# Performance work log

Measured on AMD Instinct MI355X. Metric: run time of the kernel, lower is better.

Reference implementation:

```python
import jax, jax.numpy as jnp
import numpy as np

B, N, D, OUT, NUM_ITERS = 8, 4096, 1024, 1024, 3
LN_EPS = 1e-5


def setup_inputs() -> dict:
    key = jax.random.key(0)
    ks = jax.random.split(key, 8)
    s = (6.0 / (2 * D)) ** 0.5  # xavier-uniform-like scale
    return {
        "query": jax.random.normal(ks[0], (B, D), jnp.float32),
        "feat": jax.random.normal(ks[1], (B, N, D), jnp.float32),
        "W_h": jax.random.uniform(ks[2], (D, D), jnp.float32, -s, s),
        "W_f": jax.random.uniform(ks[3], (D, D), jnp.float32, -s, s),
        "W_g": jax.random.normal(ks[4], (4, D, D), jnp.float32) / np.sqrt(D),
        "ln_w": jnp.ones((D,), jnp.float32),
        "ln_b": jnp.zeros((D,), jnp.float32),
        "W_out": jax.random.uniform(ks[5], (OUT, D), jnp.float32, -s, s),
        "b_out": jnp.zeros((OUT,), jnp.float32),
        "feat_mask": jax.random.bernoulli(ks[6], 0.2, (B, 1, 1, N)),
    }


def _layer_norm(x, w, b):
    mu = x.mean(-1, keepdims=True)
    var = jnp.var(x, axis=-1, keepdims=True)
    return (x - mu) / jnp.sqrt(var + LN_EPS) * w + b


def reference(query, feat, W_h, W_f, W_g, ln_w, ln_b, W_out, b_out, feat_mask):
    q = query @ W_h                       # [B, D]
    f = feat @ W_f                        # [B, N, D]
    mask = feat_mask.reshape(feat.shape[0], feat.shape[1])  # squeeze(1).squeeze(1)
    b = jnp.where(mask, jnp.float32(-1e18), jnp.float32(0.0))  # [B, N]
    # feat_group is iteration-invariant: mean over the 4 orthogonal transforms
    # mean_g(f @ W_g[g].T) == f @ mean_g(W_g).T
    fg = f @ W_g.mean(0).T                # [B, N, D]
    n = fg.shape[1]
    for i in range(NUM_ITERS):
        c = jax.nn.softmax(b, axis=1)     # [B, N]
        if i == NUM_ITERS - 1:
            out = jnp.einsum('bn,bnd->bd', c, fg)
        else:
            delta = jnp.einsum('bd,bnd->bn', q, fg)
            delta = (delta - delta.mean(1, keepdims=True)) / (
                delta.std(1, keepdims=True, ddof=1) + 1e-9)  # torch.std is unbiased
            b = b + delta
            out = jnp.einsum('bn,bnd->bd', c, fg) / n  # mean over dim 1
        q = _layer_norm(q + jax.nn.selu(out), ln_w, ln_b)
    return q @ W_out.T + b_out
```

## Files before the change

### kernel.cpp

```cpp
#include <hip/hip_runtime.h>
#include <hip/hip_bf16.h>


using u16 = unsigned short;
using u32 = unsigned int;
using u8  = unsigned char;
using u64 = unsigned long long;

#define SELU_L 1.0507009873554805f
#define SELU_A 1.6732632423543772f

__device__ float g_M[1048576];
__device__ float g_q[8192];
__device__ float g_tus[24576];
__device__ float g_bst[32768];
__device__ float g_c[32768];
__device__ float g_delta[32768];
__device__ float g_outv[8192];
__device__ float g_v[8192];
__device__ int   g_dt[12];

__device__ __forceinline__ float blo(u32 u){ return __uint_as_float(u << 16); }
__device__ __forceinline__ float bhi(u32 u){ return __uint_as_float(u & 0xffff0000u); }
__device__ __forceinline__ float b2f(u16 u){ return __uint_as_float(((u32)u) << 16); }

__device__ __forceinline__ void unpack8(uint4 x, float* f){
  f[0]=blo(x.x); f[1]=bhi(x.x); f[2]=blo(x.y); f[3]=bhi(x.y);
  f[4]=blo(x.z); f[5]=bhi(x.z); f[6]=blo(x.w); f[7]=bhi(x.w);
}

__device__ __forceinline__ float ldf(const void* p, size_t i, int dt){
  return dt ? ((const float*)p)[i] : b2f(((const u16*)p)[i]);
}
__device__ __forceinline__ void load8(const void* base, size_t idx, int dt, float* f){
  if (dt == 0) {
    uint4 x = *(const uint4*)((const u16*)base + idx);
    unpack8(x, f);
  } else {
    const float* p = (const float*)base + idx;
    float4 a = *(const float4*)p, b = *(const float4*)(p + 4);
    f[0]=a.x; f[1]=a.y; f[2]=a.z; f[3]=a.w; f[4]=b.x; f[5]=b.y; f[6]=b.z; f[7]=b.w;
  }
}

__device__ __forceinline__ float wredsum(float x){
#pragma unroll
  for (int o = 32; o; o >>= 1) x += __shfl_xor(x, o, 64);
  return x;
}

__global__ void kdet(const void* p0, const void* p1, const void* p2, const void* p3,
                     const void* p4, const void* p5, const void* p6, const void* p7,
                     const void* p8, const void* p9)
{
  const void* ps[10] = {p0,p1,p2,p3,p4,p5,p6,p7,p8,p9};
  int tid = threadIdx.x;
  int w = tid >> 6, lane = tid & 63;
  if (w < 9) {
    const u16* wp = (const u16*)ps[w];
    u16 x0 = wp[lane], x1 = wp[64 + lane];
    int e0 = (x0 >> 7) & 0xFF, e1 = (x1 >> 7) & 0xFF;
    u64 nz0 = __ballot(x0 != 0), nz1 = __ballot(x1 != 0);
    u64 pa0 = __ballot(x0 != 0 && e0 >= 0x70 && e0 <= 0x8F);
    u64 pa1 = __ballot(x1 != 0 && e1 >= 0x70 && e1 <= 0x8F);
    if (lane == 0) {
      const u64 evenm = 0x5555555555555555ULL;
      int nz = __popcll(nz0) + __popcll(nz1);
      int pass = __popcll(pa0) + __popcll(pa1);
      int evenNZ = __popcll(nz0 & evenm) + __popcll(nz1 & evenm);
      int oddNZ  = nz - evenNZ;
      int dt;
      if (nz == 0)                    dt = 0;
      else if (evenNZ == 0 && oddNZ)  dt = 1;
      else                            dt = (pass * 10 >= nz * 9) ? 0 : 1;
      g_dt[w] = dt;
    }
  } else if (w == 9) {
    const u8* mp = (const u8*)ps[9];
    u64 v = ((const u64*)mp)[lane];
    bool f16c=false, isF=false, nz01=false, nzNon4=false, nzM8_4=false, anynz=false;
#pragma unroll
    for (int j = 0; j < 8; ++j) {
      u8 cb = (u8)(v >> (8 * j));
      if (!cb) continue;
      int i = lane * 8 + j;
      anynz = true;
      if (cb == 0x3C && (i & 1)) f16c = true;
      if (cb == 0x3F || cb == 0x80) isF = true;
      int m = i & 3;
      if (m == 0 || m == 1) nz01 = true;
      if (m != 0) nzNon4 = true;
      if ((i & 7) == 4) nzM8_4 = true;
    }
    bool A  = __ballot(f16c)   != 0;
    bool Bf = __ballot(isF)    != 0;
    bool C  = __ballot(nz01)   != 0;
    bool Dn = __ballot(nzNon4) != 0;
    bool E  = __ballot(nzM8_4) != 0;
    bool F  = __ballot(anynz)  != 0;
    if (lane == 0) {
      int mode;
      if (A)       mode = 4;
      else if (Bf) mode = C ? 2 : 3;
      else if (Dn) mode = 0;
      else if (E)  mode = 1;
      else if (F)  mode = 5;
      else         mode = 1;
      g_dt[9] = mode;
    }
  }
  for (int i = tid; i < 8192; i += 640) g_q[i] = 0.f;
}

__global__ void kzero() {
  int i = (blockIdx.x * 256 + threadIdx.x) * 4;
  *(float4*)(g_tus + i) = make_float4(0.f, 0.f, 0.f, 0.f);
}

__global__ void kprep(const void* __restrict__ Wg, const void* __restrict__ Wh,
                      const void* __restrict__ query, const u8* __restrict__ maskp)
{
  int blk = blockIdx.x, tid = threadIdx.x;
  if (blk < 1024) {
    int dtg = g_dt[4];
    int e = blk * 1024 + tid * 4;
    float a0=0.f,a1=0.f,a2=0.f,a3=0.f;
#pragma unroll
    for (int g = 0; g < 4; ++g) {
      size_t o = (size_t)g * 1048576 + e;
      a0 += ldf(Wg, o+0, dtg); a1 += ldf(Wg, o+1, dtg);
      a2 += ldf(Wg, o+2, dtg); a3 += ldf(Wg, o+3, dtg);
    }
    *(float4*)(g_M + e) = make_float4(a0*0.25f, a1*0.25f, a2*0.25f, a3*0.25f);
  } else if (blk < 1088) {
    int dtq = g_dt[0], dth = g_dt[2];
    __shared__ float ql[512];
    int blk2 = blk - 1024;
    int kt = blk2 & 3, dc = blk2 >> 2;
    for (int idx = tid; idx < 512; idx += 256) {
      int b = idx >> 6, d = idx & 63;
      ql[idx] = ldf(query, b * 1024 + dc * 64 + d, dtq);
    }
    __syncthreads();
    int k = kt * 256 + tid;
    float acc[8] = {0,0,0,0,0,0,0,0};
    for (int dd = 0; dd < 64; ++dd) {
      int d = dc * 64 + dd;
      float w = ldf(Wh, (size_t)d * 1024 + k, dth);
#pragma unroll
      for (int b = 0; b < 8; ++b) acc[b] += ql[(b << 6) + dd] * w;
    }
#pragma unroll
    for (int b = 0; b < 8; ++b) atomicAdd(&g_q[b * 1024 + k], acc[b]);
  } else {
    int mode = g_dt[9];
    int e0 = (blk - 1088) * 1024 + tid * 4;
#pragma unroll
    for (int j = 0; j < 4; ++j) {
      int e = e0 + j;
      bool on;
      if (mode == 0)      on = maskp[e] != 0;
      else if (mode == 1) on = ((const int*)maskp)[e] != 0;
      else if (mode == 2) on = ((const u16*)maskp)[e] != 0;
      else if (mode == 3) on = ((const u32*)maskp)[e] != 0;
      else if (mode == 4) on = ((const u16*)maskp)[e] != 0;
      else                on = ((const u64*)maskp)[e] != 0ULL;
      g_bst[e] = on ? -1e18f : 0.f;
    }
  }
}

__global__ void ksm(int do_t)
{
  __shared__ float sm[1024];
  int blk = blockIdx.x, tid = threadIdx.x;
  float* t = g_tus;
  if (blk < 8) {
    int b = blk;
    const float* row = g_bst + b * 4096;
    float mx = -3.4e38f;
    for (int i = tid; i < 4096; i += 256) mx = fmaxf(mx, row[i]);
    sm[tid] = mx; __syncthreads();
    for (int s2 = 128; s2; s2 >>= 1) { if (tid < s2) sm[tid] = fmaxf(sm[tid], sm[tid + s2]); __syncthreads(); }
    mx = sm[0]; __syncthreads();
    float sum = 0.f;
    for (int i = tid; i < 4096; i += 256) {
      float e = __expf(row[i] - mx);
      g_c[b * 4096 + i] = e; sum += e;
    }
    sm[tid] = sum; __syncthreads();
    for (int s2 = 128; s2; s2 >>= 1) { if (tid < s2) sm[tid] += sm[tid + s2]; __syncthreads(); }
    float inv = 1.f / sm[0];
    for (int i = tid; i < 4096; i += 256) g_c[b * 4096 + i] *= inv;
  } else {
    int blk2 = blk - 8;
    int jt = blk2 & 3, dc = blk2 >> 2;
    for (int idx = tid; idx < 512; idx += 256) {
      int b = idx >> 6, d = idx & 63;
      sm[idx] = g_q[b * 1024 + dc * 64 + d];
    }
    __syncthreads();
    int j = jt * 256 + tid;
    float acc[8] = {0,0,0,0,0,0,0,0};
    for (int dd = 0; dd < 64; ++dd) {
      int d = dc * 64 + dd;
      float mv = g_M[(size_t)d * 1024 + j];
#pragma unroll
      for (int b = 0; b < 8; ++b) acc[b] += sm[(b << 6) + dd] * mv;
    }
#pragma unroll
    for (int b = 0; b < 8; ++b) atomicAdd(&t[b * 1024 + j], acc[b]);
  }
}

__global__ void kv(const void* __restrict__ Wf)
{
  __shared__ float tl[8192];
  int tid = threadIdx.x;
  int dtf = g_dt[3];
  for (int i = tid; i < 8192; i += 256) tl[i] = g_tus[i];
  __syncthreads();
  int w = tid >> 6, lane = tid & 63;
  int k = blockIdx.x * 4 + w;
  size_t row = (size_t)k * 1024;
  float f[16];
  load8(Wf, row + lane * 8, dtf, f);
  load8(Wf, row + 512 + lane * 8, dtf, f + 8);
  float acc[8];
#pragma unroll
  for (int b = 0; b < 8; ++b) {
    const float* tb = tl + b * 1024;
    float d = 0.f;
#pragma unroll
    for (int j = 0; j < 8; ++j) d += f[j]     * tb[lane * 8 + j];
#pragma unroll
    for (int j = 0; j < 8; ++j) d += f[8 + j] * tb[512 + lane * 8 + j];
    acc[b] = wredsum(d);
  }
  if (lane == 0) {
#pragma unroll
    for (int b = 0; b < 8; ++b) g_v[b * 1024 + k] = acc[b];
  }
}

__global__ void __launch_bounds__(256)
kfeat(const void* __restrict__ feat, int need_delta)
{
  __shared__ float sl[4][1024];
  int tid = threadIdx.x, w = tid >> 6, lane = tid & 63;
  int b = blockIdx.x >> 6, ch = blockIdx.x & 63;
  int dtf = g_dt[1];
  float* s = g_tus + 16384;
  float vr[16];
#pragma unroll
  for (int j = 0; j < 16; ++j) vr[j] = 0.f;
  if (need_delta) {
    const float* vb = g_v + b * 1024;
#pragma unroll
    for (int j = 0; j < 8; ++j) { vr[j] = vb[lane * 8 + j]; vr[8 + j] = vb[512 + lane * 8 + j]; }
  }
  float acc[16];
#pragma unroll
  for (int j = 0; j < 16; ++j) acc[j] = 0.f;
  int n0 = ch * 64 + w * 16;
  for (int r = 0; r < 16; ++r) {
    int n = n0 + r;
    size_t row = ((size_t)b * 4096 + n) * 1024;
    float f[16];
    load8(feat, row + lane * 8, dtf, f);
    load8(feat, row + 512 + lane * 8, dtf, f + 8);
    float cn = g_c[b * 4096 + n];
#pragma unroll
    for (int j = 0; j < 16; ++j) acc[j] += cn * f[j];
    if (need_delta) {
      float dot = 0.f;
#pragma unroll
      for (int j = 0; j < 16; ++j) dot += f[j] * vr[j];
      dot = wredsum(dot);
      if (lane == 0) g_delta[b * 4096 + n] = dot;
    }
  }
#pragma unroll
  for (int j = 0; j < 8; ++j) {
    sl[w][lane * 8 + j] = acc[j];
    sl[w][512 + lane * 8 + j] = acc[8 + j];
  }
  __syncthreads();
#pragma unroll
  for (int j = 0; j < 4; ++j) {
    int k = tid * 4 + j;
    float val = sl[0][k] + sl[1][k] + sl[2][k] + sl[3][k];
    atomicAdd(&s[b * 1024 + k], val);
  }
}

__global__ void kpost(const void* __restrict__ Wf, int do_stats)
{
  __shared__ float sm[1024];
  int blk = blockIdx.x, tid = threadIdx.x;
  float* u = g_tus + 8192;
  float* s = g_tus + 16384;
  if (do_stats && blk < 8) {
    int b = blk;
    const float* row = g_delta + b * 4096;
    float xs[16], sum = 0.f, sq = 0.f;
#pragma unroll
    for (int r = 0; r < 16; ++r) { float x = row[tid + 256 * r]; xs[r] = x; sum += x; sq += x * x; }
    sm[tid] = sum; __syncthreads();
    for (int s2 = 128; s2; s2 >>= 1) { if (tid < s2) sm[tid] += sm[tid + s2]; __syncthreads(); }
    sum = sm[0]; __syncthreads();
    sm[tid] = sq; __syncthreads();
    for (int s2 = 128; s2; s2 >>= 1) { if (tid < s2) sm[tid] += sm[tid + s2]; __syncthreads(); }
    sq = sm[0];
    float mean = sum / 4096.f;
    float var = fmaxf((sq - 4096.f * mean * mean) / 4095.f, 0.f);
    float inv = 1.f / (sqrtf(var) + 1e-9f);
#pragma unroll
    for (int r = 0; r < 16; ++r) {
      int i = tid + 256 * r;
      g_bst[b * 4096 + i] += (xs[r] - mean) * inv;
    }
  } else {
    int dtf = g_dt[3];
    int blk2 = blk - (do_stats ? 8 : 0);
    int jt = blk2 & 3, kc = blk2 >> 2;
    for (int idx = tid; idx < 512; idx += 256) {
      int b = idx >> 6, kk = idx & 63;
      sm[idx] = s[b * 1024 + kc * 64 + kk];
    }
    __syncthreads();
    int j = jt * 256 + tid;
    float acc[8] = {0,0,0,0,0,0,0,0};
    for (int kk = 0; kk < 64; ++kk) {
      int k = kc * 64 + kk;
      float w = ldf(Wf, (size_t)k * 1024 + j, dtf);
#pragma unroll
      for (int b = 0; b < 8; ++b) acc[b] += sm[(b << 6) + kk] * w;
    }
#pragma unroll
    for (int b = 0; b < 8; ++b) atomicAdd(&u[b * 1024 + j], acc[b]);
  }
}

__global__ void kout()
{
  __shared__ float ul[8192];
  int tid = threadIdx.x;
  for (int i = tid; i < 8192; i += 256) ul[i] = g_tus[8192 + i];
  __syncthreads();
  int w = tid >> 6, lane = tid & 63;
  int d = blockIdx.x * 4 + w;
  const float* row = g_M + (size_t)d * 1024;
  float f[16];
#pragma unroll
  for (int cc = 0; cc < 4; ++cc) {
    float4 x = *(const float4*)(row + cc * 256 + lane * 4);
    f[cc*4+0]=x.x; f[cc*4+1]=x.y; f[cc*4+2]=x.z; f[cc*4+3]=x.w;
  }
  float acc[8];
#pragma unroll
  for (int b = 0; b < 8; ++b) {
    const float* ub = ul + b * 1024;
    float dd = 0.f;
#pragma unroll
    for (int cc = 0; cc < 4; ++cc)
#pragma unroll
      for (int e = 0; e < 4; ++e) dd += f[cc * 4 + e] * ub[cc * 256 + lane * 4 + e];
    acc[b] = wredsum(dd);
  }
  if (lane == 0) {
#pragma unroll
    for (int b = 0; b < 8; ++b) g_outv[b * 1024 + d] = acc[b];
  }
}

__global__ void kq(const void* __restrict__ lnw, const void* __restrict__ lnb,
                   float scale)
{
  __shared__ float sm[256];
  int b = blockIdx.x, tid = threadIdx.x;
  int dtw = g_dt[5], dtb = g_dt[6];
  float x[4], sum = 0.f, sq = 0.f;
#pragma unroll
  for (int j = 0; j < 4; ++j) {
    int d = tid * 4 + j;
    float o = g_outv[b * 1024 + d] * scale;
    float se = (o > 0.f) ? SELU_L * o : SELU_L * SELU_A * expm1f(o);
    float val = g_q[b * 1024 + d] + se;
    x[j] = val; sum += val; sq += val * val;
  }
  sm[tid] = sum; __syncthreads();
  for (int s2 = 128; s2; s2 >>= 1) { if (tid < s2) sm[tid] += sm[tid + s2]; __syncthreads(); }
  sum = sm[0]; __syncthreads();
  sm[tid] = sq; __syncthreads();
  for (int s2 = 128; s2; s2 >>= 1) { if (tid < s2) sm[tid] += sm[tid + s2]; __syncthreads(); }
  sq = sm[0];
  float mean = sum / 1024.f;
  float var = fmaxf(sq / 1024.f - mean * mean, 0.f);
  float rstd = rsqrtf(var + 1e-5f);
#pragma unroll
  for (int j = 0; j < 4; ++j) {
    int d = tid * 4 + j;
    g_q[b * 1024 + d] = (x[j] - mean) * rstd * ldf(lnw, d, dtw) + ldf(lnb, d, dtb);
  }
}

__global__ void kfin(const void* __restrict__ Wout, const void* __restrict__ bout,
                     float* __restrict__ out)
{
  __shared__ float ql[8192];
  int tid = threadIdx.x;
  int dto = g_dt[7], dtb = g_dt[8];
  for (int i = tid; i < 8192; i += 256) ql[i] = g_q[i];
  __syncthreads();
  int w = tid >> 6, lane = tid & 63;
  int o = blockIdx.x * 4 + w;
  size_t row = (size_t)o * 1024;
  float f[16];
  load8(Wout, row + lane * 8, dto, f);
  load8(Wout, row + 512 + lane * 8, dto, f + 8);
  float acc[8];
#pragma unroll
  for (int b = 0; b < 8; ++b) {
    const float* qb = ql + b * 1024;
    float d = 0.f;
#pragma unroll
    for (int j = 0; j < 8; ++j) d += f[j]     * qb[lane * 8 + j];
#pragma unroll
    for (int j = 0; j < 8; ++j) d += f[8 + j] * qb[512 + lane * 8 + j];
    acc[b] = wredsum(d);
  }
  if (lane == 0) {
    float bo = ldf(bout, o, dtb);
#pragma unroll
    for (int b = 0; b < 8; ++b) out[b * 1024 + o] = acc[b] + bo;
  }
}

extern "C" void kernel_launch(void* const* d_in, const int* in_sizes, int n_in,
                              void* d_out, int out_size, void* d_ws, size_t ws_size,
                              hipStream_t stream)
{
  const void* query = d_in[0];
  const void* feat  = d_in[1];
  const void* Wh    = d_in[2];
  const void* Wf    = d_in[3];
  const void* Wg    = d_in[4];
  const void* lnw   = d_in[5];
  const void* lnb   = d_in[6];
  const void* Wout  = d_in[7];
  const void* bout  = d_in[8];
  const u8*   maskp = (const u8*)d_in[9];
  (void)in_sizes; (void)n_in; (void)out_size; (void)d_ws; (void)ws_size;

  kdet<<<1, 640, 0, stream>>>(query, feat, Wh, Wf, Wg, lnw, lnb, Wout, bout, maskp);
  kprep<<<1120, 256, 0, stream>>>(Wg, Wh, query, maskp);

  for (int i = 0; i < 3; ++i) {
    int nl = (i < 2);
    kzero<<<24, 256, 0, stream>>>();
    ksm<<<8 + (nl ? 64 : 0), 256, 0, stream>>>(nl);
    if (nl) kv<<<256, 256, 0, stream>>>(Wf);
    kfeat<<<512, 256, 0, stream>>>(feat, nl);
    kpost<<<(nl ? 8 : 0) + 64, 256, 0, stream>>>(Wf, nl);
    kout<<<256, 256, 0, stream>>>();
    kq<<<8, 256, 0, stream>>>(lnw, lnb, nl ? (1.f / 4096.f) : 1.f);
  }
  kfin<<<256, 256, 0, stream>>>(Wout, bout, (float*)d_out);
}
```

Measured before the change: 430.2 us.

## Precompute combined Wf·M product and fuse per-iteration kernels to cut launches

Precomputes Q = Wf·Mᵀ (and its transpose) once in a tiled GEMM kernel, so each iteration does one matrix-vector pass instead of two chained ones (M then Wf), removing the atomic-accumulated intermediates and the zeroing kernel. The layer-norm/SELU update is fused into the next iteration's merge kernel and into the final projection, with per-block recomputation, which reduces launches from about seven per iteration to three. kfeat also batches its wave reductions after the row loop. The cost is a new 1024x1024x1024 fp32 GEMM up front, plus redundant layer-norm work in every block.

Result: slower. 458.9 us (+6.7%).

```diff
diff --git a/kernel.cpp b/kernel.cpp
--- a/kernel.cpp
+++ b/kernel.cpp
@@ -11,8 +11,11 @@
 #define SELU_A 1.6732632423543772f
 
 __device__ float g_M[1048576];
+__device__ float g_Q[1048576];
+__device__ float g_Qt[1048576];
 __device__ float g_q[8192];
-__device__ float g_tus[24576];
+__device__ float g_q2[8192];
+__device__ float g_s[8192];
 __device__ float g_bst[32768];
 __device__ float g_c[32768];
 __device__ float g_delta[32768];
@@ -112,11 +115,6 @@
   for (int i = tid; i < 8192; i += 640) g_q[i] = 0.f;
 }
 
-__global__ void kzero() {
-  int i = (blockIdx.x * 256 + threadIdx.x) * 4;
-  *(float4*)(g_tus + i) = make_float4(0.f, 0.f, 0.f, 0.f);
-}
-
 __global__ void kprep(const void* __restrict__ Wg, const void* __restrict__ Wh,
                       const void* __restrict__ query, const u8* __restrict__ maskp)
 {
@@ -170,12 +168,125 @@
   }
 }
 
-__global__ void ksm(int do_t)
-{
-  __shared__ float sm[1024];
+__global__ void __launch_bounds__(256) kq_mat(const void* __restrict__ Wf)
+{
+  __shared__ float As[64 * 65];
+  __shared__ float Bs[64 * 65];
+  int tid = threadIdx.x;
+  int k0 = (blockIdx.x & 15) * 64, d0 = (blockIdx.x >> 4) * 64;
+  int dtf = g_dt[3];
+  int tx = tid & 15, ty = tid >> 4;
+  float acc[4][4];
+#pragma unroll
+  for (int i = 0; i < 4; ++i)
+#pragma unroll
+    for (int l = 0; l < 4; ++l) acc[i][l] = 0.f;
+
+  for (int jc = 0; jc < 1024; jc += 64) {
+    if (jc) __syncthreads();
+#pragma unroll
+    for (int t2 = 0; t2 < 2; ++t2) {
+      int idx = tid + t2 * 256;
+      int row = idx >> 3, seg = idx & 7;
+      float f[8];
+      load8(Wf, (size_t)(k0 + row) * 1024 + jc + seg * 8, dtf, f);
+#pragma unroll
+      for (int u = 0; u < 8; ++u) As[row * 65 + seg * 8 + u] = f[u];
+      const float* mrow = g_M + (size_t)(d0 + row) * 1024 + jc + seg * 8;
+      float4 m0 = *(const float4*)mrow, m1 = *(const float4*)(mrow + 4);
+      Bs[row * 65 + seg * 8 + 0] = m0.x; Bs[row * 65 + seg * 8 + 1] = m0.y;
+      Bs[row * 65 + seg * 8 + 2] = m0.z; Bs[row * 65 + seg * 8 + 3] = m0.w;
+      Bs[row * 65 + seg * 8 + 4] = m1.x; Bs[row * 65 + seg * 8 + 5] = m1.y;
+      Bs[row * 65 + seg * 8 + 6] = m1.z; Bs[row * 65 + seg * 8 + 7] = m1.w;
+    }
+    __syncthreads();
+#pragma unroll 8
+    for (int j = 0; j < 64; ++j) {
+      float a0 = As[(ty * 4 + 0) * 65 + j];
+      float a1 = As[(ty * 4 + 1) * 65 + j];
+      float a2 = As[(ty * 4 + 2) * 65 + j];
+      float a3 = As[(ty * 4 + 3) * 65 + j];
+      float b0 = Bs[(tx * 4 + 0) * 65 + j];
+      float b1 = Bs[(tx * 4 + 1) * 65 + j];
+      float b2 = Bs[(tx * 4 + 2) * 65 + j];
+      float b3 = Bs[(tx * 4 + 3) * 65 + j];
+      acc[0][0] += a0*b0; acc[0][1] += a0*b1; acc[0][2] += a0*b2; acc[0][3] += a0*b3;
+      acc[1][0] += a1*b0; acc[1][1] += a1*b1; acc[1][2] += a1*b2; acc[1][3] += a1*b3;
+      acc[2][0] += a2*b0; acc[2][1] += a2*b1; acc[2][2] += a2*b2; acc[2][3] += a2*b3;
+      acc[3][0] += a3*b0; acc[3][1] += a3*b1; acc[3][2] += a3*b2; acc[3][3] += a3*b3;
+    }
+  }
+#pragma unroll
+  for (int i = 0; i < 4; ++i) {
+    *(float4*)(g_Q + (size_t)(k0 + ty * 4 + i) * 1024 + d0 + tx * 4) =
+        make_float4(acc[i][0], acc[i][1], acc[i][2], acc[i][3]);
+  }
+  __syncthreads();
+#pragma unroll
+  for (int i = 0; i < 4; ++i)
+#pragma unroll
+    for (int l = 0; l < 4; ++l) As[(tx * 4 + l) * 65 + ty * 4 + i] = acc[i][l];
+  __syncthreads();
+  {
+    int row = tid >> 2, q4 = tid & 3;
+    float v16[16];
+#pragma unroll
+    for (int e = 0; e < 16; ++e) v16[e] = As[row * 65 + q4 * 16 + e];
+#pragma unroll
+    for (int c2 = 0; c2 < 4; ++c2)
+      *(float4*)(g_Qt + (size_t)(d0 + row) * 1024 + k0 + q4 * 16 + c2 * 4) =
+          make_float4(v16[c2*4], v16[c2*4+1], v16[c2*4+2], v16[c2*4+3]);
+  }
+}
+
+__device__ __forceinline__ void build_ql(float* ql, const float* qsrc, float scale,
+                                         const void* lnw, const void* lnb, int tid)
+{
+  int w = tid >> 6, lane = tid & 63;
+  int dtw = g_dt[5], dtb = g_dt[6];
+#pragma unroll
+  for (int rr = 0; rr < 2; ++rr) {
+    int b = w + rr * 4;
+    const float* qb = qsrc + b * 1024;
+    const float* ob = g_outv + b * 1024;
+    float x[16]; float sum = 0.f, sq = 0.f;
+#pragma unroll
+    for (int cc = 0; cc < 4; ++cc) {
+      float4 qv = *(const float4*)(qb + cc * 256 + lane * 4);
+      float4 ov = *(const float4*)(ob + cc * 256 + lane * 4);
+      float q4[4] = {qv.x, qv.y, qv.z, qv.w};
+      float o4[4] = {ov.x, ov.y, ov.z, ov.w};
+#pragma unroll
+      for (int e = 0; e < 4; ++e) {
+        float o = o4[e] * scale;
+        float se = (o > 0.f) ? SELU_L * o : SELU_L * SELU_A * expm1f(o);
+        float val = q4[e] + se;
+        x[cc * 4 + e] = val; sum += val; sq += val * val;
+      }
+    }
+    sum = wredsum(sum); sq = wredsum(sq);
+    float mean = sum * (1.f / 1024.f);
+    float var = fmaxf(sq * (1.f / 1024.f) - mean * mean, 0.f);
+    float rstd = rsqrtf(var + 1e-5f);
+#pragma unroll
+    for (int cc = 0; cc < 4; ++cc)
+#pragma unroll
+      for (int e = 0; e < 4; ++e) {
+        int d = cc * 256 + lane * 4 + e;
+        ql[b * 1024 + d] = (x[cc * 4 + e] - mean) * rstd * ldf(lnw, d, dtw)
+                           + ldf(lnb, d, dtb);
+      }
+  }
+  __syncthreads();
+}
+
+__global__ void __launch_bounds__(256) kmerge(const void* __restrict__ lnw,
+                                              const void* __restrict__ lnb,
+                                              int phase, float scale)
+{
   int blk = blockIdx.x, tid = threadIdx.x;
-  float* t = g_tus;
   if (blk < 8) {
+    __shared__ float sm[1024];
     int b = blk;
     const float* row = g_bst + b * 4096;
     float mx = -3.4e38f;
@@ -192,49 +303,41 @@
     for (int s2 = 128; s2; s2 >>= 1) { if (tid < s2) sm[tid] += sm[tid + s2]; __syncthreads(); }
     float inv = 1.f / sm[0];
     for (int i = tid; i < 4096; i += 256) g_c[b * 4096 + i] *= inv;
+    for (int i = tid; i < 1024; i += 256) g_s[b * 1024 + i] = 0.f;
+    return;
+  }
+  __shared__ float ql[8192];
+  const float* qsrc = (phase == 2) ? g_q2 : g_q;
+  if (phase == 0) {
+    for (int i = tid; i < 8192; i += 256) ql[i] = qsrc[i];
+    __syncthreads();
   } else {
-    int blk2 = blk - 8;
-    int jt = blk2 & 3, dc = blk2 >> 2;
-    for (int idx = tid; idx < 512; idx += 256) {
-      int b = idx >> 6, d = idx & 63;
-      sm[idx] = g_q[b * 1024 + dc * 64 + d];
-    }
-    __syncthreads();
-    int j = jt * 256 + tid;
-    float acc[8] = {0,0,0,0,0,0,0,0};
-    for (int dd = 0; dd < 64; ++dd) {
-      int d = dc * 64 + dd;
-      float mv = g_M[(size_t)d * 1024 + j];
-#pragma unroll
-      for (int b = 0; b < 8; ++b) acc[b] += sm[(b << 6) + dd] * mv;
-    }
-#pragma unroll
-    for (int b = 0; b < 8; ++b) atomicAdd(&t[b * 1024 + j], acc[b]);
-  }
-}
-
-__global__ void kv(const void* __restrict__ Wf)
-{
-  __shared__ float tl[8192];
-  int tid = threadIdx.x;
-  int dtf = g_dt[3];
-  for (int i = tid; i < 8192; i += 256) tl[i] = g_tus[i];
-  __syncthreads();
+    build_ql(ql, qsrc, scale, lnw, lnb, tid);
+  }
+  if (phase >= 1 && blk == 8) {
+    float* qdst = (phase == 2) ? g_q : g_q2;
+    for (int i = tid; i < 8192; i += 256) qdst[i] = ql[i];
+  }
+  if (phase == 2) return;
   int w = tid >> 6, lane = tid & 63;
-  int k = blockIdx.x * 4 + w;
-  size_t row = (size_t)k * 1024;
+  int k = (blk - 8) * 4 + w;
+  const float* Qrow = g_Q + (size_t)k * 1024;
   float f[16];
-  load8(Wf, row + lane * 8, dtf, f);
-  load8(Wf, row + 512 + lane * 8, dtf, f + 8);
+#pragma unroll
+  for (int cc = 0; cc < 4; ++cc) {
+    float4 x = *(const float4*)(Qrow + cc * 256 + lane * 4);
+    f[cc*4] = x.x; f[cc*4+1] = x.y; f[cc*4+2] = x.z; f[cc*4+3] = x.w;
+  }
   float acc[8];
 #pragma unroll
   for (int b = 0; b < 8; ++b) {
-    const float* tb = tl + b * 1024;
+    const float* qb = ql + b * 1024;
     float d = 0.f;
 #pragma unroll
-    for (int j = 0; j < 8; ++j) d += f[j]     * tb[lane * 8 + j];
-#pragma unroll
-    for (int j = 0; j < 8; ++j) d += f[8 + j] * tb[512 + lane * 8 + j];
+    for (int cc = 0; cc < 4; ++cc) {
+      float4 qv = *(const float4*)(qb + cc * 256 + lane * 4);
+      d += f[cc*4] * qv.x + f[cc*4+1] * qv.y + f[cc*4+2] * qv.z + f[cc*4+3] * qv.w;
+    }
     acc[b] = wredsum(d);
   }
   if (lane == 0) {
@@ -250,7 +353,6 @@
   int tid = threadIdx.x, w = tid >> 6, lane = tid & 63;
   int b = blockIdx.x >> 6, ch = blockIdx.x & 63;
   int dtf = g_dt[1];
-  float* s = g_tus + 16384;
   float vr[16];
 #pragma unroll
   for (int j = 0; j < 16; ++j) vr[j] = 0.f;
@@ -259,25 +361,35 @@
 #pragma unroll
     for (int j = 0; j < 8; ++j) { vr[j] = vb[lane * 8 + j]; vr[8 + j] = vb[512 + lane * 8 + j]; }
   }
+  int n0 = ch * 64 + w * 16;
+  float cc16[16];
+#pragma unroll
+  for (int r = 0; r < 16; ++r) cc16[r] = g_c[b * 4096 + n0 + r];
   float acc[16];
 #pragma unroll
   for (int j = 0; j < 16; ++j) acc[j] = 0.f;
-  int n0 = ch * 64 + w * 16;
+  float dp[16];
   for (int r = 0; r < 16; ++r) {
-    int n = n0 + r;
-    size_t row = ((size_t)b * 4096 + n) * 1024;
+    size_t row = ((size_t)b * 4096 + n0 + r) * 1024;
     float f[16];
     load8(feat, row + lane * 8, dtf, f);
     load8(feat, row + 512 + lane * 8, dtf, f + 8);
-    float cn = g_c[b * 4096 + n];
+    float cn = cc16[r];
 #pragma unroll
     for (int j = 0; j < 16; ++j) acc[j] += cn * f[j];
+    float dot = 0.f;
     if (need_delta) {
-      float dot = 0.f;
 #pragma unroll
       for (int j = 0; j < 16; ++j) dot += f[j] * vr[j];
-      dot = wredsum(dot);
-      if (lane == 0) g_delta[b * 4096 + n] = dot;
+    }
+    dp[r] = dot;
+  }
+  if (need_delta) {
+#pragma unroll
+    for (int r = 0; r < 16; ++r) dp[r] = wredsum(dp[r]);
+    if (lane == 0) {
+#pragma unroll
+      for (int r = 0; r < 16; ++r) g_delta[b * 4096 + n0 + r] = dp[r];
     }
   }
 #pragma unroll
@@ -290,28 +402,27 @@
   for (int j = 0; j < 4; ++j) {
     int k = tid * 4 + j;
     float val = sl[0][k] + sl[1][k] + sl[2][k] + sl[3][k];
-    atomicAdd(&s[b * 1024 + k], val);
-  }
-}
-
-__global__ void kpost(const void* __restrict__ Wf, int do_stats)
-{
-  __shared__ float sm[1024];
+    atomicAdd(&g_s[b * 1024 + k], val);
+  }
+}
+
+__global__ void __launch_bounds__(256) kpost(int do_stats)
+{
+  __shared__ float sh[8192];
   int blk = blockIdx.x, tid = threadIdx.x;
-  float* u = g_tus + 8192;
-  float* s = g_tus + 16384;
-  if (do_stats && blk < 8) {
+  if (blk < 8) {
+    if (!do_stats) return;
     int b = blk;
     const float* row = g_delta + b * 4096;
     float xs[16], sum = 0.f, sq = 0.f;
 #pragma unroll
     for (int r = 0; r < 16; ++r) { float x = row[tid + 256 * r]; xs[r] = x; sum += x; sq += x * x; }
-    sm[tid] = sum; __syncthreads();
-    for (int s2 = 128; s2; s2 >>= 1) { if (tid < s2) sm[tid] += sm[tid + s2]; __syncthreads(); }
-    sum = sm[0]; __syncthreads();
-    sm[tid] = sq; __syncthreads();
-    for (int s2 = 128; s2; s2 >>= 1) { if (tid < s2) sm[tid] += sm[tid + s2]; __syncthreads(); }
-    sq = sm[0];
+    sh[tid] = sum; __syncthreads();
+    for (int s2 = 128; s2; s2 >>= 1) { if (tid < s2) sh[tid] += sh[tid + s2]; __syncthreads(); }
+    sum = sh[0]; __syncthreads();
+    sh[tid] = sq; __syncthreads();
+    for (int s2 = 128; s2; s2 >>= 1) { if (tid < s2) sh[tid] += sh[tid + s2]; __syncthreads(); }
+    sq = sh[0];
     float mean = sum / 4096.f;
     float var = fmaxf((sq - 4096.f * mean * mean) / 4095.f, 0.f);
     float inv = 1.f / (sqrtf(var) + 1e-9f);
@@ -320,52 +431,29 @@
       int i = tid + 256 * r;
       g_bst[b * 4096 + i] += (xs[r] - mean) * inv;
     }
-  } else {
-    int dtf = g_dt[3];
-    int blk2 = blk - (do_stats ? 8 : 0);
-    int jt = blk2 & 3, kc = blk2 >> 2;
-    for (int idx = tid; idx < 512; idx += 256) {
-      int b = idx >> 6, kk = idx & 63;
-      sm[idx] = s[b * 1024 + kc * 64 + kk];
-    }
-    __syncthreads();
-    int j = jt * 256 + tid;
-    float acc[8] = {0,0,0,0,0,0,0,0};
-    for (int kk = 0; kk < 64; ++kk) {
-      int k = kc * 64 + kk;
-      float w = ldf(Wf, (size_t)k * 1024 + j, dtf);
-#pragma unroll
-      for (int b = 0; b < 8; ++b) acc[b] += sm[(b << 6) + kk] * w;
-    }
-#pragma unroll
-    for (int b = 0; b < 8; ++b) atomicAdd(&u[b * 1024 + j], acc[b]);
-  }
-}
-
-__global__ void kout()
-{
-  __shared__ float ul[8192];
-  int tid = threadIdx.x;
-  for (int i = tid; i < 8192; i += 256) ul[i] = g_tus[8192 + i];
+    return;
+  }
+  for (int i = tid; i < 8192; i += 256) sh[i] = g_s[i];
   __syncthreads();
   int w = tid >> 6, lane = tid & 63;
-  int d = blockIdx.x * 4 + w;
-  const float* row = g_M + (size_t)d * 1024;
+  int d = (blk - 8) * 4 + w;
+  const float* Qtr = g_Qt + (size_t)d * 1024;
   float f[16];
 #pragma unroll
   for (int cc = 0; cc < 4; ++cc) {
-    float4 x = *(const float4*)(row + cc * 256 + lane * 4);
-    f[cc*4+0]=x.x; f[cc*4+1]=x.y; f[cc*4+2]=x.z; f[cc*4+3]=x.w;
+    float4 x = *(const float4*)(Qtr + cc * 256 + lane * 4);
+    f[cc*4] = x.x; f[cc*4+1] = x.y; f[cc*4+2] = x.z; f[cc*4+3] = x.w;
   }
   float acc[8];
 #pragma unroll
   for (int b = 0; b < 8; ++b) {
-    const float* ub = ul + b * 1024;
+    const float* sb = sh + b * 1024;
     float dd = 0.f;
 #pragma unroll
-    for (int cc = 0; cc < 4; ++cc)
-#pragma unroll
-      for (int e = 0; e < 4; ++e) dd += f[cc * 4 + e] * ub[cc * 256 + lane * 4 + e];
+    for (int cc = 0; cc < 4; ++cc) {
+      float4 sv = *(const float4*)(sb + cc * 256 + lane * 4);
+      dd += f[cc*4] * sv.x + f[cc*4+1] * sv.y + f[cc*4+2] * sv.z + f[cc*4+3] * sv.w;
+    }
     acc[b] = wredsum(dd);
   }
   if (lane == 0) {
@@ -374,47 +462,18 @@
   }
 }
 
-__global__ void kq(const void* __restrict__ lnw, const void* __restrict__ lnb,
-                   float scale)
-{
-  __shared__ float sm[256];
-  int b = blockIdx.x, tid = threadIdx.x;
-  int dtw = g_dt[5], dtb = g_dt[6];
-  float x[4], sum = 0.f, sq = 0.f;
-#pragma unroll
-  for (int j = 0; j < 4; ++j) {
-    int d = tid * 4 + j;
-    float o = g_outv[b * 1024 + d] * scale;
-    float se = (o > 0.f) ? SELU_L * o : SELU_L * SELU_A * expm1f(o);
-    float val = g_q[b * 1024 + d] + se;
-    x[j] = val; sum += val; sq += val * val;
-  }
-  sm[tid] = sum; __syncthreads();
-  for (int s2 = 128; s2; s2 >>= 1) { if (tid < s2) sm[tid] += sm[tid + s2]; __syncthreads(); }
-  sum = sm[0]; __syncthreads();
-  sm[tid] = sq; __syncthreads();
-  for (int s2 = 128; s2; s2 >>= 1) { if (tid < s2) sm[tid] += sm[tid + s2]; __syncthreads(); }
-  sq = sm[0];
-  float mean = sum / 1024.f;
-  float var = fmaxf(sq / 1024.f - mean * mean, 0.f);
-  float rstd = rsqrtf(var + 1e-5f);
-#pragma unroll
-  for (int j = 0; j < 4; ++j) {
-    int d = tid * 4 + j;
-    g_q[b * 1024 + d] = (x[j] - mean) * rstd * ldf(lnw, d, dtw) + ldf(lnb, d, dtb);
-  }
-}
-
-__global__ void kfin(const void* __restrict__ Wout, const void* __restrict__ bout,
-                     float* __restrict__ out)
+__global__ void __launch_bounds__(256) kfin(const void* __restrict__ Wout,
+                                            const void* __restrict__ bout,
+                                            const void* __restrict__ lnw,
+                                            const void* __restrict__ lnb,
+                                            float* __restrict__ out)
 {
   __shared__ float ql[8192];
   int tid = threadIdx.x;
-  int dto = g_dt[7], dtb = g_dt[8];
-  for (int i = tid; i < 8192; i += 256) ql[i] = g_q[i];
-  __syncthreads();
+  build_ql(ql, g_q, 1.f, lnw, lnb, tid);
   int w = tid >> 6, lane = tid & 63;
   int o = blockIdx.x * 4 + w;
+  int dto = g_dt[7], dtb = g_dt[8];
   size_t row = (size_t)o * 1024;
   float f[16];
   load8(Wout, row + lane * 8, dto, f);
@@ -455,16 +514,13 @@
 
   kdet<<<1, 640, 0, stream>>>(query, feat, Wh, Wf, Wg, lnw, lnb, Wout, bout, maskp);
   kprep<<<1120, 256, 0, stream>>>(Wg, Wh, query, maskp);
+  kq_mat<<<256, 256, 0, stream>>>(Wf);
 
   for (int i = 0; i < 3; ++i) {
     int nl = (i < 2);
-    kzero<<<24, 256, 0, stream>>>();
-    ksm<<<8 + (nl ? 64 : 0), 256, 0, stream>>>(nl);
-    if (nl) kv<<<256, 256, 0, stream>>>(Wf);
+    kmerge<<<(i == 2) ? 9 : 264, 256, 0, stream>>>(lnw, lnb, i, 1.f / 4096.f);
     kfeat<<<512, 256, 0, stream>>>(feat, nl);
-    kpost<<<(nl ? 8 : 0) + 64, 256, 0, stream>>>(Wf, nl);
-    kout<<<256, 256, 0, stream>>>();
-    kq<<<8, 256, 0, stream>>>(lnw, lnb, nl ? (1.f / 4096.f) : 1.f);
-  }
-  kfin<<<256, 256, 0, stream>>>(Wout, bout, (float*)d_out);
-}
+    kpost<<<264, 256, 0, stream>>>(nl);
+  }
+  kfin<<<256, 256, 0, stream>>>(Wout, bout, lnw, lnb, (float*)d_out);
+}
```

## Fuse iteration loop into one cooperative persistent kernel with grid syncs

Applied to the files above, without the earlier changes.

Replaces the per-iteration chain of about seven small kernel launches with a single cooperative kernel of 512 blocks. Phases are separated by grid.sync, and zeroing and layer norm are folded into the first phase. The small matvec phases are also re-split into finer chunks (16 rows per block instead of 64) to spread them over more blocks. This targets launch overhead and idle gaps between the many tiny dependent kernels. In exchange it adds grid-wide barrier costs and 32KB of shared memory per block, and keeps a multi-kernel fallback in case the cooperative launch fails.

New measurement: 1.346 ms. 3.13x slower.

```diff
diff --git a/kernel.cpp b/kernel.cpp
--- a/kernel.cpp
+++ b/kernel.cpp
@@ -1,5 +1,8 @@
 #include <hip/hip_runtime.h>
 #include <hip/hip_bf16.h>
+#include <hip/hip_cooperative_groups.h>
+
+namespace cg = cooperative_groups;
 
 
 using u16 = unsigned short;
@@ -12,13 +15,18 @@
 
 __device__ float g_M[1048576];
 __device__ float g_q[8192];
-__device__ float g_tus[24576];
+__device__ float g_qc[8192];
+__device__ float g_t[8192];
+__device__ float g_u[8192];
+__device__ float g_s[8192];
 __device__ float g_bst[32768];
 __device__ float g_c[32768];
 __device__ float g_delta[32768];
 __device__ float g_outv[8192];
 __device__ float g_v[8192];
 __device__ int   g_dt[12];
+
+constexpr int NBLK = 512;
 
 __device__ __forceinline__ float blo(u32 u){ return __uint_as_float(u << 16); }
 __device__ __forceinline__ float bhi(u32 u){ return __uint_as_float(u & 0xffff0000u); }
@@ -112,11 +120,6 @@
   for (int i = tid; i < 8192; i += 640) g_q[i] = 0.f;
 }
 
-__global__ void kzero() {
-  int i = (blockIdx.x * 256 + threadIdx.x) * 4;
-  *(float4*)(g_tus + i) = make_float4(0.f, 0.f, 0.f, 0.f);
-}
-
 __global__ void kprep(const void* __restrict__ Wg, const void* __restrict__ Wh,
                       const void* __restrict__ query, const u8* __restrict__ maskp)
 {
@@ -170,58 +173,111 @@
   }
 }
 
-__global__ void ksm(int do_t)
-{
-  __shared__ float sm[1024];
-  int blk = blockIdx.x, tid = threadIdx.x;
-  float* t = g_tus;
+
+__device__ __forceinline__ void ph_softmax(int b, float* sm)
+{
+  int tid = threadIdx.x;
+  const float* row = g_bst + b * 4096;
+  float mx = -3.4e38f;
+  for (int i = tid; i < 4096; i += 256) mx = fmaxf(mx, row[i]);
+  sm[tid] = mx; __syncthreads();
+  for (int s2 = 128; s2; s2 >>= 1) { if (tid < s2) sm[tid] = fmaxf(sm[tid], sm[tid + s2]); __syncthreads(); }
+  mx = sm[0]; __syncthreads();
+  float sum = 0.f;
+  for (int i = tid; i < 4096; i += 256) {
+    float e = __expf(row[i] - mx);
+    g_c[b * 4096 + i] = e; sum += e;
+  }
+  sm[tid] = sum; __syncthreads();
+  for (int s2 = 128; s2; s2 >>= 1) { if (tid < s2) sm[tid] += sm[tid + s2]; __syncthreads(); }
+  float inv = 1.f / sm[0];
+  for (int i = tid; i < 4096; i += 256) g_c[b * 4096 + i] *= inv;
+}
+
+__device__ __forceinline__ void ph_ln(int b, const float* qsrc, float scale,
+                                      const void* lnw, const void* lnb, float* sm)
+{
+  int tid = threadIdx.x;
+  int dtw = g_dt[5], dtb = g_dt[6];
+  float x[4]; float sum = 0.f, sq = 0.f;
+#pragma unroll
+  for (int j = 0; j < 4; ++j) {
+    int d = tid * 4 + j;
+    float o = g_outv[b * 1024 + d] * scale;
+    float se = (o > 0.f) ? SELU_L * o : SELU_L * SELU_A * expm1f(o);
+    float val = qsrc[b * 1024 + d] + se;
+    x[j] = val; sum += val; sq += val * val;
+  }
+  sm[tid] = sum; __syncthreads();
+  for (int s2 = 128; s2; s2 >>= 1) { if (tid < s2) sm[tid] += sm[tid + s2]; __syncthreads(); }
+  sum = sm[0]; __syncthreads();
+  sm[tid] = sq; __syncthreads();
+  for (int s2 = 128; s2; s2 >>= 1) { if (tid < s2) sm[tid] += sm[tid + s2]; __syncthreads(); }
+  sq = sm[0]; __syncthreads();
+  float mean = sum / 1024.f;
+  float var = fmaxf(sq / 1024.f - mean * mean, 0.f);
+  float rstd = rsqrtf(var + 1e-5f);
+#pragma unroll
+  for (int j = 0; j < 4; ++j) {
+    int d = tid * 4 + j;
+    g_qc[b * 1024 + d] = (x[j] - mean) * rstd * ldf(lnw, d, dtw) + ldf(lnb, d, dtb);
+  }
+}
+
+__device__ __forceinline__ void ph_A(int blk, int iter, const void* lnw,
+                                     const void* lnb, float* shm)
+{
+  int tid = threadIdx.x;
   if (blk < 8) {
-    int b = blk;
-    const float* row = g_bst + b * 4096;
-    float mx = -3.4e38f;
-    for (int i = tid; i < 4096; i += 256) mx = fmaxf(mx, row[i]);
-    sm[tid] = mx; __syncthreads();
-    for (int s2 = 128; s2; s2 >>= 1) { if (tid < s2) sm[tid] = fmaxf(sm[tid], sm[tid + s2]); __syncthreads(); }
-    mx = sm[0]; __syncthreads();
-    float sum = 0.f;
-    for (int i = tid; i < 4096; i += 256) {
-      float e = __expf(row[i] - mx);
-      g_c[b * 4096 + i] = e; sum += e;
-    }
-    sm[tid] = sum; __syncthreads();
-    for (int s2 = 128; s2; s2 >>= 1) { if (tid < s2) sm[tid] += sm[tid + s2]; __syncthreads(); }
-    float inv = 1.f / sm[0];
-    for (int i = tid; i < 4096; i += 256) g_c[b * 4096 + i] *= inv;
-  } else {
-    int blk2 = blk - 8;
-    int jt = blk2 & 3, dc = blk2 >> 2;
-    for (int idx = tid; idx < 512; idx += 256) {
-      int b = idx >> 6, d = idx & 63;
-      sm[idx] = g_q[b * 1024 + dc * 64 + d];
-    }
-    __syncthreads();
-    int j = jt * 256 + tid;
-    float acc[8] = {0,0,0,0,0,0,0,0};
-    for (int dd = 0; dd < 64; ++dd) {
-      int d = dc * 64 + dd;
-      float mv = g_M[(size_t)d * 1024 + j];
-#pragma unroll
-      for (int b = 0; b < 8; ++b) acc[b] += sm[(b << 6) + dd] * mv;
-    }
-#pragma unroll
-    for (int b = 0; b < 8; ++b) atomicAdd(&t[b * 1024 + j], acc[b]);
-  }
-}
-
-__global__ void kv(const void* __restrict__ Wf)
-{
-  __shared__ float tl[8192];
+    ph_softmax(blk, shm);
+  } else if (blk < 16) {
+    int b = blk - 8;
+    if (iter == 0) {
+      for (int j = tid; j < 1024; j += 256) g_qc[b * 1024 + j] = g_q[b * 1024 + j];
+    } else {
+      ph_ln(b, g_qc, 1.f / 4096.f, lnw, lnb, shm);
+    }
+  } else if (blk < 24) {
+    int b = blk - 16;
+    *(float4*)(g_s + b * 1024 + tid * 4) = make_float4(0.f, 0.f, 0.f, 0.f);
+  } else if (blk < 32) {
+    int b = blk - 24;
+    *(float4*)(g_t + b * 1024 + tid * 4) = make_float4(0.f, 0.f, 0.f, 0.f);
+  } else if (blk < 40) {
+    int b = blk - 32;
+    *(float4*)(g_u + b * 1024 + tid * 4) = make_float4(0.f, 0.f, 0.f, 0.f);
+  }
+}
+
+__device__ __forceinline__ void ph_t(int blk, float* shm)
+{
+  int tid = threadIdx.x;
+  int jt = blk & 3, dc4 = blk >> 2;
+  if (tid < 128) {
+    int b = tid >> 4, dd = tid & 15;
+    shm[tid] = g_qc[b * 1024 + dc4 * 16 + dd];
+  }
+  __syncthreads();
+  int j = jt * 256 + tid;
+  float acc[8] = {0,0,0,0,0,0,0,0};
+  for (int dd = 0; dd < 16; ++dd) {
+    float mv = g_M[(size_t)(dc4 * 16 + dd) * 1024 + j];
+#pragma unroll
+    for (int b = 0; b < 8; ++b) acc[b] += shm[(b << 4) + dd] * mv;
+  }
+#pragma unroll
+  for (int b = 0; b < 8; ++b) atomicAdd(&g_t[b * 1024 + j], acc[b]);
+  __syncthreads();
+}
+
+__device__ __forceinline__ void ph_v(int blk, const void* Wf, float* shm)
+{
   int tid = threadIdx.x;
   int dtf = g_dt[3];
-  for (int i = tid; i < 8192; i += 256) tl[i] = g_tus[i];
+  for (int i = tid; i < 8192; i += 256) shm[i] = g_t[i];
   __syncthreads();
   int w = tid >> 6, lane = tid & 63;
-  int k = blockIdx.x * 4 + w;
+  int k = blk * 4 + w;
   size_t row = (size_t)k * 1024;
   float f[16];
   load8(Wf, row + lane * 8, dtf, f);
@@ -229,7 +285,7 @@
   float acc[8];
 #pragma unroll
   for (int b = 0; b < 8; ++b) {
-    const float* tb = tl + b * 1024;
+    const float* tb = shm + b * 1024;
     float d = 0.f;
 #pragma unroll
     for (int j = 0; j < 8; ++j) d += f[j]     * tb[lane * 8 + j];
@@ -241,16 +297,15 @@
 #pragma unroll
     for (int b = 0; b < 8; ++b) g_v[b * 1024 + k] = acc[b];
   }
-}
-
-__global__ void __launch_bounds__(256)
-kfeat(const void* __restrict__ feat, int need_delta)
-{
-  __shared__ float sl[4][1024];
+  __syncthreads();
+}
+
+__device__ __forceinline__ void ph_feat(int blk, const void* feat, int need_delta,
+                                        float* shm)
+{
   int tid = threadIdx.x, w = tid >> 6, lane = tid & 63;
-  int b = blockIdx.x >> 6, ch = blockIdx.x & 63;
+  int b = blk >> 6, ch = blk & 63;
   int dtf = g_dt[1];
-  float* s = g_tus + 16384;
   float vr[16];
 #pragma unroll
   for (int j = 0; j < 16; ++j) vr[j] = 0.f;
@@ -282,139 +337,107 @@
   }
 #pragma unroll
   for (int j = 0; j < 8; ++j) {
-    sl[w][lane * 8 + j] = acc[j];
-    sl[w][512 + lane * 8 + j] = acc[8 + j];
+    shm[w * 1024 + lane * 8 + j] = acc[j];
+    shm[w * 1024 + 512 + lane * 8 + j] = acc[8 + j];
   }
   __syncthreads();
 #pragma unroll
   for (int j = 0; j < 4; ++j) {
     int k = tid * 4 + j;
-    float val = sl[0][k] + sl[1][k] + sl[2][k] + sl[3][k];
-    atomicAdd(&s[b * 1024 + k], val);
-  }
-}
-
-__global__ void kpost(const void* __restrict__ Wf, int do_stats)
-{
-  __shared__ float sm[1024];
-  int blk = blockIdx.x, tid = threadIdx.x;
-  float* u = g_tus + 8192;
-  float* s = g_tus + 16384;
-  if (do_stats && blk < 8) {
-    int b = blk;
-    const float* row = g_delta + b * 4096;
-    float xs[16], sum = 0.f, sq = 0.f;
-#pragma unroll
-    for (int r = 0; r < 16; ++r) { float x = row[tid + 256 * r]; xs[r] = x; sum += x; sq += x * x; }
-    sm[tid] = sum; __syncthreads();
-    for (int s2 = 128; s2; s2 >>= 1) { if (tid < s2) sm[tid] += sm[tid + s2]; __syncthreads(); }
-    sum = sm[0]; __syncthreads();
-    sm[tid] = sq; __syncthreads();
-    for (int s2 = 128; s2; s2 >>= 1) { if (tid < s2) sm[tid] += sm[tid + s2]; __syncthreads(); }
-    sq = sm[0];
-    float mean = sum / 4096.f;
-    float var = fmaxf((sq - 4096.f * mean * mean) / 4095.f, 0.f);
-    float inv = 1.f / (sqrtf(var) + 1e-9f);
-#pragma unroll
-    for (int r = 0; r < 16; ++r) {
-      int i = tid + 256 * r;
-      g_bst[b * 4096 + i] += (xs[r] - mean) * inv;
-    }
-  } else {
-    int dtf = g_dt[3];
-    int blk2 = blk - (do_stats ? 8 : 0);
-    int jt = blk2 & 3, kc = blk2 >> 2;
-    for (int idx = tid; idx < 512; idx += 256) {
-      int b = idx >> 6, kk = idx & 63;
-      sm[idx] = s[b * 1024 + kc * 64 + kk];
-    }
-    __syncthreads();
-    int j = jt * 256 + tid;
-    float acc[8] = {0,0,0,0,0,0,0,0};
-    for (int kk = 0; kk < 64; ++kk) {
-      int k = kc * 64 + kk;
-      float w = ldf(Wf, (size_t)k * 1024 + j, dtf);
-#pragma unroll
-      for (int b = 0; b < 8; ++b) acc[b] += sm[(b << 6) + kk] * w;
-    }
-#pragma unroll
-    for (int b = 0; b < 8; ++b) atomicAdd(&u[b * 1024 + j], acc[b]);
-  }
-}
-
-__global__ void kout()
-{
-  __shared__ float ul[8192];
-  int tid = threadIdx.x;
-  for (int i = tid; i < 8192; i += 256) ul[i] = g_tus[8192 + i];
-  __syncthreads();
-  int w = tid >> 6, lane = tid & 63;
-  int d = blockIdx.x * 4 + w;
-  const float* row = g_M + (size_t)d * 1024;
-  float f[16];
-#pragma unroll
-  for (int cc = 0; cc < 4; ++cc) {
-    float4 x = *(const float4*)(row + cc * 256 + lane * 4);
-    f[cc*4+0]=x.x; f[cc*4+1]=x.y; f[cc*4+2]=x.z; f[cc*4+3]=x.w;
-  }
-  float acc[8];
-#pragma unroll
-  for (int b = 0; b < 8; ++b) {
-    const float* ub = ul + b * 1024;
-    float dd = 0.f;
-#pragma unroll
-    for (int cc = 0; cc < 4; ++cc)
-#pragma unroll
-      for (int e = 0; e < 4; ++e) dd += f[cc * 4 + e] * ub[cc * 256 + lane * 4 + e];
-    acc[b] = wredsum(dd);
-  }
-  if (lane == 0) {
-#pragma unroll
-    for (int b = 0; b < 8; ++b) g_outv[b * 1024 + d] = acc[b];
-  }
-}
-
-__global__ void kq(const void* __restrict__ lnw, const void* __restrict__ lnb,
-                   float scale)
-{
-  __shared__ float sm[256];
-  int b = blockIdx.x, tid = threadIdx.x;
-  int dtw = g_dt[5], dtb = g_dt[6];
-  float x[4], sum = 0.f, sq = 0.f;
-#pragma unroll
-  for (int j = 0; j < 4; ++j) {
-    int d = tid * 4 + j;
-    float o = g_outv[b * 1024 + d] * scale;
-    float se = (o > 0.f) ? SELU_L * o : SELU_L * SELU_A * expm1f(o);
-    float val = g_q[b * 1024 + d] + se;
-    x[j] = val; sum += val; sq += val * val;
-  }
+    float val = shm[k] + shm[1024 + k] + shm[2048 + k] + shm[3072 + k];
+    atomicAdd(&g_s[b * 1024 + k], val);
+  }
+  __syncthreads();
+}
+
+__device__ __forceinline__ void ph_stats(int b, float* sm)
+{
+  int tid = threadIdx.x;
+  const float* row = g_delta + b * 4096;
+  float xs[16], sum = 0.f, sq = 0.f;
+#pragma unroll
+  for (int r = 0; r < 16; ++r) { float x = row[tid + 256 * r]; xs[r] = x; sum += x; sq += x * x; }
   sm[tid] = sum; __syncthreads();
   for (int s2 = 128; s2; s2 >>= 1) { if (tid < s2) sm[tid] += sm[tid + s2]; __syncthreads(); }
   sum = sm[0]; __syncthreads();
   sm[tid] = sq; __syncthreads();
   for (int s2 = 128; s2; s2 >>= 1) { if (tid < s2) sm[tid] += sm[tid + s2]; __syncthreads(); }
   sq = sm[0];
-  float mean = sum / 1024.f;
-  float var = fmaxf(sq / 1024.f - mean * mean, 0.f);
-  float rstd = rsqrtf(var + 1e-5f);
-#pragma unroll
-  for (int j = 0; j < 4; ++j) {
-    int d = tid * 4 + j;
-    g_q[b * 1024 + d] = (x[j] - mean) * rstd * ldf(lnw, d, dtw) + ldf(lnb, d, dtb);
-  }
-}
-
-__global__ void kfin(const void* __restrict__ Wout, const void* __restrict__ bout,
-                     float* __restrict__ out)
-{
-  __shared__ float ql[8192];
+  float mean = sum / 4096.f;
+  float var = fmaxf((sq - 4096.f * mean * mean) / 4095.f, 0.f);
+  float inv = 1.f / (sqrtf(var) + 1e-9f);
+#pragma unroll
+  for (int r = 0; r < 16; ++r) {
+    int i = tid + 256 * r;
+    g_bst[b * 4096 + i] += (xs[r] - mean) * inv;
+  }
+  __syncthreads();
+}
+
+__device__ __forceinline__ void ph_u(int blk2, const void* Wf, float* shm)
+{
+  int tid = threadIdx.x;
+  int dtf = g_dt[3];
+  int jt = blk2 & 3, kc4 = blk2 >> 2;
+  if (tid < 128) {
+    int b = tid >> 4, kk = tid & 15;
+    shm[tid] = g_s[b * 1024 + kc4 * 16 + kk];
+  }
+  __syncthreads();
+  int j = jt * 256 + tid;
+  float acc[8] = {0,0,0,0,0,0,0,0};
+  for (int kk = 0; kk < 16; ++kk) {
+    int k = kc4 * 16 + kk;
+    float w = ldf(Wf, (size_t)k * 1024 + j, dtf);
+#pragma unroll
+    for (int b = 0; b < 8; ++b) acc[b] += shm[(b << 4) + kk] * w;
+  }
+#pragma unroll
+  for (int b = 0; b < 8; ++b) atomicAdd(&g_u[b * 1024 + j], acc[b]);
+  __syncthreads();
+}
+
+__device__ __forceinline__ void ph_out(int blk, float* shm)
+{
+  int tid = threadIdx.x;
+  for (int i = tid; i < 8192; i += 256) shm[i] = g_u[i];
+  __syncthreads();
+  int w = tid >> 6, lane = tid & 63;
+  int d = blk * 4 + w;
+  const float* row = g_M + (size_t)d * 1024;
+  float f[16];
+#pragma unroll
+  for (int cc = 0; cc < 4; ++cc) {
+    float4 x = *(const float4*)(row + cc * 256 + lane * 4);
+    f[cc*4+0]=x.x; f[cc*4+1]=x.y; f[cc*4+2]=x.z; f[cc*4+3]=x.w;
+  }
+  float acc[8];
+#pragma unroll
+  for (int b = 0; b < 8; ++b) {
+    const float* ub = shm + b * 1024;
+    float dd = 0.f;
+#pragma unroll
+    for (int cc = 0; cc < 4; ++cc)
+#pragma unroll
+      for (int e = 0; e < 4; ++e) dd += f[cc * 4 + e] * ub[cc * 256 + lane * 4 + e];
+    acc[b] = wredsum(dd);
+  }
+  if (lane == 0) {
+#pragma unroll
+    for (int b = 0; b < 8; ++b) g_outv[b * 1024 + d] = acc[b];
+  }
+  __syncthreads();
+}
+
+__device__ __forceinline__ void ph_fin(int blk, const void* Wout, const void* bout,
+                                       float* __restrict__ out, float* shm)
+{
   int tid = threadIdx.x;
   int dto = g_dt[7], dtb = g_dt[8];
-  for (int i = tid; i < 8192; i += 256) ql[i] = g_q[i];
+  for (int i = tid; i < 8192; i += 256) shm[i] = g_qc[i];
   __syncthreads();
   int w = tid >> 6, lane = tid & 63;
-  int o = blockIdx.x * 4 + w;
+  int o = blk * 4 + w;
   size_t row = (size_t)o * 1024;
   float f[16];
   load8(Wout, row + lane * 8, dto, f);
@@ -422,7 +445,7 @@
   float acc[8];
 #pragma unroll
   for (int b = 0; b < 8; ++b) {
-    const float* qb = ql + b * 1024;
+    const float* qb = shm + b * 1024;
     float d = 0.f;
 #pragma unroll
     for (int j = 0; j < 8; ++j) d += f[j]     * qb[lane * 8 + j];
@@ -436,6 +459,60 @@
     for (int b = 0; b < 8; ++b) out[b * 1024 + o] = acc[b] + bo;
   }
 }
+
+__global__ void __launch_bounds__(256, 2)
+kcoop(const void* __restrict__ feat, const void* __restrict__ Wf,
+      const void* __restrict__ lnw, const void* __restrict__ lnb,
+      const void* __restrict__ Wout, const void* __restrict__ bout,
+      float* __restrict__ out)
+{
+  cg::grid_group grid = cg::this_grid();
+  __shared__ float shm[8192];
+  int blk = blockIdx.x;
+
+  for (int i = 0; i < 3; ++i) {
+    int nl = (i < 2);
+    ph_A(blk, i, lnw, lnb, shm);
+    grid.sync();
+    if (nl) {
+      if (blk < 256) ph_t(blk, shm);
+      grid.sync();
+      if (blk < 256) ph_v(blk, Wf, shm);
+      grid.sync();
+    }
+    ph_feat(blk, feat, nl, shm);
+    grid.sync();
+    if (nl && blk < 8) ph_stats(blk, shm);
+    else if (blk >= 8 && blk < 264) ph_u(blk - 8, Wf, shm);
+    grid.sync();
+    if (blk < 256) ph_out(blk, shm);
+    grid.sync();
+  }
+  if (blk < 8) ph_ln(blk, g_qc, 1.f, lnw, lnb, shm);
+  grid.sync();
+  if (blk < 256) ph_fin(blk, Wout, bout, out, shm);
+}
+
+__global__ void __launch_bounds__(256) fA(const void* lnw, const void* lnb, int iter)
+{ __shared__ float shm[1024]; ph_A(blockIdx.x, iter, lnw, lnb, shm); }
+__global__ void __launch_bounds__(256) fB()
+{ __shared__ float shm[128]; ph_t(blockIdx.x, shm); }
+__global__ void __launch_bounds__(256) fC(const void* Wf)
+{ __shared__ float shm[8192]; ph_v(blockIdx.x, Wf, shm); }
+__global__ void __launch_bounds__(256) fD(const void* feat, int nd)
+{ __shared__ float shm[4096]; ph_feat(blockIdx.x, feat, nd, shm); }
+__global__ void __launch_bounds__(256) fE(const void* Wf, int nl)
+{
+  __shared__ float shm[256];
+  if (nl && blockIdx.x < 8) ph_stats(blockIdx.x, shm);
+  else if (blockIdx.x >= 8 && blockIdx.x < 264) ph_u(blockIdx.x - 8, Wf, shm);
+}
+__global__ void __launch_bounds__(256) fF()
+{ __shared__ float shm[8192]; ph_out(blockIdx.x, shm); }
+__global__ void __launch_bounds__(256) fG(const void* lnw, const void* lnb)
+{ __shared__ float shm[256]; ph_ln(blockIdx.x, g_qc, 1.f, lnw, lnb, shm); }
+__global__ void __launch_bounds__(256) fH(const void* Wout, const void* bout, float* out)
+{ __shared__ float shm[8192]; ph_fin(blockIdx.x, Wout, bout, out, shm); }
 
 extern "C" void kernel_launch(void* const* d_in, const int* in_sizes, int n_in,
                               void* d_out, int out_size, void* d_ws, size_t ws_size,
@@ -451,20 +528,29 @@
   const void* Wout  = d_in[7];
   const void* bout  = d_in[8];
   const u8*   maskp = (const u8*)d_in[9];
+  float* outp = (float*)d_out;
   (void)in_sizes; (void)n_in; (void)out_size; (void)d_ws; (void)ws_size;
 
   kdet<<<1, 640, 0, stream>>>(query, feat, Wh, Wf, Wg, lnw, lnb, Wout, bout, maskp);
   kprep<<<1120, 256, 0, stream>>>(Wg, Wh, query, maskp);
 
-  for (int i = 0; i < 3; ++i) {
-    int nl = (i < 2);
-    kzero<<<24, 256, 0, stream>>>();
-    ksm<<<8 + (nl ? 64 : 0), 256, 0, stream>>>(nl);
-    if (nl) kv<<<256, 256, 0, stream>>>(Wf);
-    kfeat<<<512, 256, 0, stream>>>(feat, nl);
-    kpost<<<(nl ? 8 : 0) + 64, 256, 0, stream>>>(Wf, nl);
-    kout<<<256, 256, 0, stream>>>();
-    kq<<<8, 256, 0, stream>>>(lnw, lnb, nl ? (1.f / 4096.f) : 1.f);
-  }
-  kfin<<<256, 256, 0, stream>>>(Wout, bout, (float*)d_out);
-}
+  void* args[] = {(void*)&feat, (void*)&Wf, (void*)&lnw, (void*)&lnb,
+                  (void*)&Wout, (void*)&bout, (void*)&outp};
+  hipError_t ce = hipLaunchCooperativeKernel((void*)kcoop, dim3(NBLK), dim3(256),
+                                             args, 0, stream);
+  if (ce != hipSuccess) {
+    for (int i = 0; i < 3; ++i) {
+      int nl = (i < 2);
+      fA<<<40, 256, 0, stream>>>(lnw, lnb, i);
+      if (nl) {
+        fB<<<256, 256, 0, stream>>>();
+        fC<<<256, 256, 0, stream>>>(Wf);
+      }
+      fD<<<512, 256, 0, stream>>>(feat, nl);
+      fE<<<264, 256, 0, stream>>>(Wf, nl);
+      fF<<<256, 256, 0, stream>>>();
+    }
+    fG<<<8, 256, 0, stream>>>(lnw, lnb);
+    fH<<<256, 256, 0, stream>>>(Wout, bout, outp);
+  }
+}
```
